# Optimization experiments

Measured on AMD Instinct MI355X. Metric: run time of the kernel, lower is better.

Reference implementation:

```python
import jax, jax.numpy as jnp
import numpy as np

TAU = 2.0       # spikingjelly LIFNode default
V_TH = 1.0      # v_threshold default
ALPHA = 2.0     # surrogate.ATan default alpha

@jax.custom_vjp
def atan_spike(x):
    # Heaviside forward, ATan surrogate gradient backward
    return (x >= 0.0).astype(x.dtype)

def _atan_fwd(x):
    return atan_spike(x), x

def _atan_bwd(x, g):
    return (g * (ALPHA / 2.0) / (1.0 + (jnp.pi / 2.0 * ALPHA * x) ** 2),)

atan_spike.defvjp(_atan_fwd, _atan_bwd)

def lif_scan(cur):
    # cur: [T, ...]; LIF with decay_input=True, hard reset to v_reset=0
    def step(v, c):
        v = v + (c - v) / TAU          # charge with decayed input
        s = atan_spike(v - V_TH)       # fire
        v = (1.0 - s) * v              # hard reset (v_reset = 0)
        return v, s
    v0 = jnp.zeros(cur.shape[1:], cur.dtype)
    _, spikes = jax.lax.scan(step, v0, cur)
    return spikes

def setup_inputs() -> dict:
    key = jax.random.key(0)
    k1, k2 = jax.random.split(key, 2)
    T, B, D = 2048, 32, 512
    x = jax.random.normal(k1, (T, B, D), dtype=jnp.float32)
    W = jax.random.normal(k2, (D, D), dtype=jnp.float32) / np.sqrt(D).astype(np.float32)
    b = jnp.zeros((D,), dtype=jnp.float32)
    return {"x": x, "W": W, "b": b}

def reference(x, W, b):
    # x: [T, B, D]
    xs = jnp.stack([x, jnp.flip(x, axis=0)], axis=2)          # [T, B, 2, D]
    cur = jnp.einsum('tbkd,ed->tbke', xs, W) + b              # Linear (y = x W^T + b)
    s = lif_scan(cur)                                          # [T, B, 2, D] spikes
    return s[:, :, 0, :] + jnp.flip(s[:, :, 1, :], axis=0)    # [T, B, D]
```

## Files before the change

### kernel.cpp

```cpp
#include <hip/hip_runtime.h>
#include <cstddef>
#include <cstdint>

#define T_LEN 2048
#define B_SZ  32
#define D_SZ  512
#define BD    (B_SZ * D_SZ)

#define BM  128
#define BN  128
#define LDP 20

__global__ __launch_bounds__(256) void gemm8x8_kernel(
    const float* __restrict__ A,
    const float* __restrict__ W,
    const float* __restrict__ bias,
    float* __restrict__ Y)
{
#pragma clang fp contract(off)
  __shared__ float As[BM][LDP];
  __shared__ float Bs[BN][LDP];

  const int tid = threadIdx.x;
  const int tx  = tid & 15;
  const int ty  = tid >> 4;
  const int m0  = blockIdx.x * BM;
  const int n0  = blockIdx.y * BN;

  const int sr = tid >> 2;
  const int sq = (tid & 3) << 2;

  const float* Ap0 = A + (size_t)(m0 + sr)      * D_SZ + sq;
  const float* Ap1 = A + (size_t)(m0 + 64 + sr) * D_SZ + sq;
  const float* Wp0 = W + (size_t)(n0 + sr)      * D_SZ + sq;
  const float* Wp1 = W + (size_t)(n0 + 64 + sr) * D_SZ + sq;

  float acc[8][8];
#pragma unroll
  for (int i = 0; i < 8; ++i)
#pragma unroll
    for (int j = 0; j < 8; ++j) acc[i][j] = 0.0f;

  float4 pa0 = *(const float4*)(Ap0);
  float4 pa1 = *(const float4*)(Ap1);
  float4 pb0 = *(const float4*)(Wp0);
  float4 pb1 = *(const float4*)(Wp1);

#pragma unroll 1
  for (int k0 = 0; k0 < D_SZ; k0 += 16) {
    __syncthreads();
    *(float4*)&As[sr][sq]      = pa0;
    *(float4*)&As[64 + sr][sq] = pa1;
    *(float4*)&Bs[sr][sq]      = pb0;
    *(float4*)&Bs[64 + sr][sq] = pb1;
    __syncthreads();

    if (k0 + 16 < D_SZ) {
      pa0 = *(const float4*)(Ap0 + k0 + 16);
      pa1 = *(const float4*)(Ap1 + k0 + 16);
      pb0 = *(const float4*)(Wp0 + k0 + 16);
      pb1 = *(const float4*)(Wp1 + k0 + 16);
    }

#pragma unroll
    for (int kq = 0; kq < 4; ++kq) {
      float4 b[8];
#pragma unroll
      for (int j = 0; j < 8; ++j)
        b[j] = *(const float4*)&Bs[tx + 16 * j][kq << 2];
#pragma unroll
      for (int i = 0; i < 8; ++i) {
        const float4 a = *(const float4*)&As[ty + 16 * i][kq << 2];
#pragma unroll
        for (int j = 0; j < 8; ++j) {
          acc[i][j] = fmaf(a.x, b[j].x, acc[i][j]);
          acc[i][j] = fmaf(a.y, b[j].y, acc[i][j]);
          acc[i][j] = fmaf(a.z, b[j].z, acc[i][j]);
          acc[i][j] = fmaf(a.w, b[j].w, acc[i][j]);
        }
      }
    }
  }

#pragma unroll
  for (int i = 0; i < 8; ++i) {
    const int m = m0 + ty + 16 * i;
#pragma unroll
    for (int j = 0; j < 8; ++j) {
      const int n = n0 + tx + 16 * j;
      Y[(size_t)m * D_SZ + n] = acc[i][j] + bias[n];
    }
  }
}

__global__ __launch_bounds__(64) void scan_dirs_kernel(
    const float* __restrict__ Y,
    uint32_t* __restrict__ bits_f,
    uint32_t* __restrict__ bits_b)
{
#pragma clang fp contract(off)
  const int blk = blockIdx.x;
  const bool fwd = blk < 256;
  const int idx = ((fwd ? blk : blk - 256) << 6) + threadIdx.x;
  float v = 0.0f;

  if (fwd) {
#pragma unroll 1
    for (int g = 0; g < 64; ++g) {
      float c[32];
#pragma unroll
      for (int j = 0; j < 32; ++j)
        c[j] = Y[(size_t)(g * 32 + j) * BD + idx];
      uint32_t w = 0;
#pragma unroll
      for (int j = 0; j < 32; ++j) {
        v = v + (c[j] - v) * 0.5f;
        const bool s = (v - 1.0f) >= 0.0f;
        w |= (uint32_t)s << j;
        v = s ? 0.0f : v;
      }
      bits_f[g * BD + idx] = w;
    }
  } else {
#pragma unroll 1
    for (int g = 63; g >= 0; --g) {
      float c[32];
#pragma unroll
      for (int j = 0; j < 32; ++j)
        c[j] = Y[(size_t)(g * 32 + j) * BD + idx];
      uint32_t w = 0;
#pragma unroll
      for (int j = 31; j >= 0; --j) {
        v = v + (c[j] - v) * 0.5f;
        const bool s = (v - 1.0f) >= 0.0f;
        w |= (uint32_t)s << j;
        v = s ? 0.0f : v;
      }
      bits_b[g * BD + idx] = w;
    }
  }
}

__global__ __launch_bounds__(256) void combine_kernel(
    const uint32_t* __restrict__ bf,
    const uint32_t* __restrict__ bb,
    float* __restrict__ out)
{
  const int gid = blockIdx.x * 256 + threadIdx.x;
  const int f0  = gid << 2;
  const int t   = f0 / BD;
  const int i0  = f0 & (BD - 1);
  const int g   = t >> 5;
  const int bit = t & 31;
  const uint4 wf = *(const uint4*)(bf + g * BD + i0);
  const uint4 wb = *(const uint4*)(bb + g * BD + i0);
  float4 r;
  r.x = (float)(((wf.x >> bit) & 1u) + ((wb.x >> bit) & 1u));
  r.y = (float)(((wf.y >> bit) & 1u) + ((wb.y >> bit) & 1u));
  r.z = (float)(((wf.z >> bit) & 1u) + ((wb.z >> bit) & 1u));
  r.w = (float)(((wf.w >> bit) & 1u) + ((wb.w >> bit) & 1u));
  *(float4*)(out + (size_t)f0) = r;
}

__global__ __launch_bounds__(64) void lif_fwd_kernel(
    const float* __restrict__ Y, float* __restrict__ out,
    int tlen, float* __restrict__ vstate, int carry)
{
#pragma clang fp contract(off)
  const int idx = blockIdx.x * 64 + threadIdx.x;
  float v = carry ? vstate[idx] : 0.0f;
#pragma unroll 16
  for (int t = 0; t < tlen; ++t) {
    const float c = Y[(size_t)t * BD + idx];
    v = v + (c - v) * 0.5f;
    const bool s = (v - 1.0f) >= 0.0f;
    out[(size_t)t * BD + idx] = s ? 1.0f : 0.0f;
    v = s ? 0.0f : v;
  }
  vstate[idx] = v;
}

__global__ __launch_bounds__(64) void lif_bwd_kernel(
    const float* __restrict__ Y, float* __restrict__ out,
    int tlen, float* __restrict__ vstate, int carry)
{
#pragma clang fp contract(off)
  const int idx = blockIdx.x * 64 + threadIdx.x;
  float v = carry ? vstate[idx] : 0.0f;
#pragma unroll 16
  for (int tt = 0; tt < tlen; ++tt) {
    const size_t t = (size_t)(tlen - 1 - tt);
    const float c = Y[t * BD + idx];
    v = v + (c - v) * 0.5f;
    const bool s = (v - 1.0f) >= 0.0f;
    out[t * BD + idx] += s ? 1.0f : 0.0f;
    v = s ? 0.0f : v;
  }
  vstate[idx] = v;
}

extern "C" void kernel_launch(void* const* d_in, const int* in_sizes, int n_in,
                              void* d_out, int out_size, void* d_ws, size_t ws_size,
                              hipStream_t stream)
{
  const float* x = (const float*)d_in[0];
  const float* W = (const float*)d_in[1];
  const float* b = (const float*)d_in[2];
  float* out = (float*)d_out;

  const size_t full_bytes = (size_t)T_LEN * BD * sizeof(float);
  const size_t bit_bytes  = (size_t)(T_LEN / 32) * BD * sizeof(uint32_t);
  const size_t vbytes     = (size_t)BD * sizeof(float);

  if (ws_size >= full_bytes + 2 * bit_bytes) {
    float*    Y  = (float*)d_ws;
    uint32_t* bf = (uint32_t*)((char*)d_ws + full_bytes);
    uint32_t* bb = (uint32_t*)((char*)d_ws + full_bytes + bit_bytes);
    dim3 grid(T_LEN * B_SZ / BM, D_SZ / BN);
    gemm8x8_kernel<<<grid, 256, 0, stream>>>(x, W, b, Y);
    scan_dirs_kernel<<<512, 64, 0, stream>>>(Y, bf, bb);
    combine_kernel<<<(T_LEN * BD / 4) / 256, 256, 0, stream>>>(bf, bb, out);
  } else if (ws_size >= full_bytes + vbytes) {
    float* Y      = (float*)d_ws;
    float* vstate = (float*)((char*)d_ws + full_bytes);
    dim3 grid(T_LEN * B_SZ / BM, D_SZ / BN);
    gemm8x8_kernel<<<grid, 256, 0, stream>>>(x, W, b, Y);
    lif_fwd_kernel<<<BD / 64, 64, 0, stream>>>(Y, out, T_LEN, vstate, 0);
    lif_bwd_kernel<<<BD / 64, 64, 0, stream>>>(Y, out, T_LEN, vstate, 0);
  } else {
    const size_t avail = ws_size > vbytes ? ws_size - vbytes : 0;
    int Tc = T_LEN;
    while (Tc > 4 && (size_t)Tc * BD * sizeof(float) > avail) Tc >>= 1;
    float* Y      = (float*)d_ws;
    float* vstate = (float*)((char*)d_ws + (size_t)Tc * BD * sizeof(float));

    int first = 1;
    for (int t0 = 0; t0 < T_LEN; t0 += Tc) {
      dim3 grid(Tc * B_SZ / BM, D_SZ / BN);
      gemm8x8_kernel<<<grid, 256, 0, stream>>>(x + (size_t)t0 * BD, W, b, Y);
      lif_fwd_kernel<<<BD / 64, 64, 0, stream>>>(Y, out + (size_t)t0 * BD, Tc,
                                                 vstate, first ? 0 : 1);
      first = 0;
    }
    first = 1;
    for (int t0 = T_LEN - Tc; t0 >= 0; t0 -= Tc) {
      dim3 grid(Tc * B_SZ / BM, D_SZ / BN);
      gemm8x8_kernel<<<grid, 256, 0, stream>>>(x + (size_t)t0 * BD, W, b, Y);
      lif_bwd_kernel<<<BD / 64, 64, 0, stream>>>(Y, out + (size_t)t0 * BD, Tc,
                                                 vstate, first ? 0 : 1);
      first = 0;
    }
  }
}
```

Before: 707.3 us.

## Chunk LIF scan over time with warmup, fuse combine, double-buffer GEMM

The bidirectional LIF scan is split into 16 time chunks of 128 steps. Each chunk rebuilds its starting membrane state by running a 128-step warmup from zero over the neighbouring chunk, relying on the 0.5 decay to wash out the unknown initial state. Spikes are written straight to the output, so the separate bit-combine kernel and the bit buffers go away. This raises scan parallelism well above the previous 512 blocks of 64 threads, at the cost of reading Y redundantly during warmup and a small risk of threshold differences. The GEMM now double-buffers LDS, loads A directly into LDS with global_load_lds, and remaps block indices across the XCDs.

```diff
diff --git a/kernel.cpp b/kernel.cpp
--- a/kernel.cpp
+++ b/kernel.cpp
@@ -7,9 +7,12 @@
 #define D_SZ  512
 #define BD    (B_SZ * D_SZ)
 
-#define BM  128
-#define BN  128
-#define LDP 20
+#define BM   128
+#define BN   128
+#define LDPB 20
+
+typedef const __attribute__((address_space(1))) uint32_t* gas1_t;
+typedef __attribute__((address_space(3))) uint32_t* las3_t;
 
 __global__ __launch_bounds__(256) void gemm8x8_kernel(
     const float* __restrict__ A,
@@ -18,68 +21,90 @@
     float* __restrict__ Y)
 {
 #pragma clang fp contract(off)
-  __shared__ float As[BM][LDP];
-  __shared__ float Bs[BN][LDP];
+  __shared__ float As[2][BM * 16];
+  __shared__ float Bs[2][BN][LDPB];
 
   const int tid = threadIdx.x;
   const int tx  = tid & 15;
   const int ty  = tid >> 4;
-  const int m0  = blockIdx.x * BM;
-  const int n0  = blockIdx.y * BN;
+
+  const int nwg  = (int)(gridDim.x * gridDim.y);
+  const int orig = (int)(blockIdx.y * gridDim.x + blockIdx.x);
+  const int q    = nwg >> 3, r = nwg & 7;
+  const int xcd  = orig & 7, loc = orig >> 3;
+  const int tix  = (xcd < r ? xcd * (q + 1) : r * (q + 1) + (xcd - r) * q) + loc;
+  const int m0   = (tix >> 2) * BM;
+  const int n0   = (tix & 3) * BN;
 
   const int sr = tid >> 2;
   const int sq = (tid & 3) << 2;
-
-  const float* Ap0 = A + (size_t)(m0 + sr)      * D_SZ + sq;
-  const float* Ap1 = A + (size_t)(m0 + 64 + sr) * D_SZ + sq;
   const float* Wp0 = W + (size_t)(n0 + sr)      * D_SZ + sq;
   const float* Wp1 = W + (size_t)(n0 + 64 + sr) * D_SZ + sq;
 
+  const int lane = tid & 63;
+  const int wid  = tid >> 6;
+  const int rloc = lane >> 2;
+  const int q4   = (lane & 3) << 2;
+  const int sA0  = 2 * wid, sA1 = 2 * wid + 1;
+  const int oS0  = sA0 * 256, oS1 = sA1 * 256;
+  const float* gA0 = A + (size_t)(m0 + sA0 * 16 + rloc) * D_SZ + q4;
+  const float* gA1 = A + (size_t)(m0 + sA1 * 16 + rloc) * D_SZ + q4;
+
   float acc[8][8];
 #pragma unroll
   for (int i = 0; i < 8; ++i)
 #pragma unroll
     for (int j = 0; j < 8; ++j) acc[i][j] = 0.0f;
 
-  float4 pa0 = *(const float4*)(Ap0);
-  float4 pa1 = *(const float4*)(Ap1);
+  __builtin_amdgcn_global_load_lds((gas1_t)(const void*)gA0,
+                                   (las3_t)(void*)(&As[0][oS0]), 16, 0, 0);
+  __builtin_amdgcn_global_load_lds((gas1_t)(const void*)gA1,
+                                   (las3_t)(void*)(&As[0][oS1]), 16, 0, 0);
   float4 pb0 = *(const float4*)(Wp0);
   float4 pb1 = *(const float4*)(Wp1);
+  *(float4*)&Bs[0][sr][sq]      = pb0;
+  *(float4*)&Bs[0][64 + sr][sq] = pb1;
+  pb0 = *(const float4*)(Wp0 + 16);
+  pb1 = *(const float4*)(Wp1 + 16);
+  __syncthreads();
 
 #pragma unroll 1
-  for (int k0 = 0; k0 < D_SZ; k0 += 16) {
+  for (int kc = 0; kc < 32; ++kc) {
+    const int cur = kc & 1;
+    const int nxt = cur ^ 1;
+    if (kc + 1 < 32) {
+      const int koff = (kc + 1) * 16;
+      __builtin_amdgcn_global_load_lds((gas1_t)(const void*)(gA0 + koff),
+                                       (las3_t)(void*)(&As[nxt][oS0]), 16, 0, 0);
+      __builtin_amdgcn_global_load_lds((gas1_t)(const void*)(gA1 + koff),
+                                       (las3_t)(void*)(&As[nxt][oS1]), 16, 0, 0);
+      *(float4*)&Bs[nxt][sr][sq]      = pb0;
+      *(float4*)&Bs[nxt][64 + sr][sq] = pb1;
+      if (kc + 2 < 32) {
+        pb0 = *(const float4*)(Wp0 + (kc + 2) * 16);
+        pb1 = *(const float4*)(Wp1 + (kc + 2) * 16);
+      }
+    }
+    const float* as = &As[cur][0];
+#pragma unroll
+    for (int kq = 0; kq < 4; ++kq) {
+      float4 bfr[8];
+#pragma unroll
+      for (int j = 0; j < 8; ++j)
+        bfr[j] = *(const float4*)&Bs[cur][tx + 16 * j][kq << 2];
+#pragma unroll
+      for (int i = 0; i < 8; ++i) {
+        const float4 a = *(const float4*)&as[(ty + 16 * i) * 16 + (kq << 2)];
+#pragma unroll
+        for (int j = 0; j < 8; ++j) {
+          acc[i][j] = fmaf(a.x, bfr[j].x, acc[i][j]);
+          acc[i][j] = fmaf(a.y, bfr[j].y, acc[i][j]);
+          acc[i][j] = fmaf(a.z, bfr[j].z, acc[i][j]);
+          acc[i][j] = fmaf(a.w, bfr[j].w, acc[i][j]);
+        }
+      }
+    }
     __syncthreads();
-    *(float4*)&As[sr][sq]      = pa0;
-    *(float4*)&As[64 + sr][sq] = pa1;
-    *(float4*)&Bs[sr][sq]      = pb0;
-    *(float4*)&Bs[64 + sr][sq] = pb1;
-    __syncthreads();
-
-    if (k0 + 16 < D_SZ) {
-      pa0 = *(const float4*)(Ap0 + k0 + 16);
-      pa1 = *(const float4*)(Ap1 + k0 + 16);
-      pb0 = *(const float4*)(Wp0 + k0 + 16);
-      pb1 = *(const float4*)(Wp1 + k0 + 16);
-    }
-
-#pragma unroll
-    for (int kq = 0; kq < 4; ++kq) {
-      float4 b[8];
-#pragma unroll
-      for (int j = 0; j < 8; ++j)
-        b[j] = *(const float4*)&Bs[tx + 16 * j][kq << 2];
-#pragma unroll
-      for (int i = 0; i < 8; ++i) {
-        const float4 a = *(const float4*)&As[ty + 16 * i][kq << 2];
-#pragma unroll
-        for (int j = 0; j < 8; ++j) {
-          acc[i][j] = fmaf(a.x, b[j].x, acc[i][j]);
-          acc[i][j] = fmaf(a.y, b[j].y, acc[i][j]);
-          acc[i][j] = fmaf(a.z, b[j].z, acc[i][j]);
-          acc[i][j] = fmaf(a.w, b[j].w, acc[i][j]);
-        }
-      }
-    }
   }
 
 #pragma unroll
@@ -93,73 +118,92 @@
   }
 }
 
-__global__ __launch_bounds__(64) void scan_dirs_kernel(
+#define CHK  16
+#define CLEN 128
+
+__global__ __launch_bounds__(64) void scan_chunk_kernel(
     const float* __restrict__ Y,
-    uint32_t* __restrict__ bits_f,
-    uint32_t* __restrict__ bits_b)
-{
-#pragma clang fp contract(off)
-  const int blk = blockIdx.x;
-  const bool fwd = blk < 256;
-  const int idx = ((fwd ? blk : blk - 256) << 6) + threadIdx.x;
-  float v = 0.0f;
-
-  if (fwd) {
+    float* __restrict__ out)
+{
+#pragma clang fp contract(off)
+  const int idx = blockIdx.x * 64 + threadIdx.x;
+  const int c   = blockIdx.y;
+  const int t0  = c * CLEN;
+  float creg[32];
+  uint32_t sf0, sf1, sf2, sf3, sb0, sb1, sb2, sb3;
+  float v;
+
+#define LOAD32(TB)                                                            \
+  _Pragma("unroll")                                                           \
+  for (int j = 0; j < 32; ++j) creg[j] = Y[(size_t)((TB) + j) * BD + idx];
+
+  v = 0.0f;
+  if (c > 0) {
 #pragma unroll 1
-    for (int g = 0; g < 64; ++g) {
-      float c[32];
-#pragma unroll
-      for (int j = 0; j < 32; ++j)
-        c[j] = Y[(size_t)(g * 32 + j) * BD + idx];
-      uint32_t w = 0;
+    for (int g = 0; g < 4; ++g) {
+      LOAD32(t0 - 128 + g * 32)
 #pragma unroll
       for (int j = 0; j < 32; ++j) {
-        v = v + (c[j] - v) * 0.5f;
+        v = v + (creg[j] - v) * 0.5f;
         const bool s = (v - 1.0f) >= 0.0f;
-        w |= (uint32_t)s << j;
         v = s ? 0.0f : v;
       }
-      bits_f[g * BD + idx] = w;
-    }
-  } else {
+    }
+  }
+#define FGRP(SF, G)                                                           \
+  {                                                                           \
+    LOAD32(t0 + (G) * 32)                                                     \
+    uint32_t w = 0;                                                           \
+    _Pragma("unroll")                                                         \
+    for (int j = 0; j < 32; ++j) {                                            \
+      v = v + (creg[j] - v) * 0.5f;                                           \
+      const bool s = (v - 1.0f) >= 0.0f;                                      \
+      w |= (uint32_t)s << j;                                                  \
+      v = s ? 0.0f : v;                                                       \
+    }                                                                         \
+    SF = w;                                                                   \
+  }
+  FGRP(sf0, 0) FGRP(sf1, 1) FGRP(sf2, 2) FGRP(sf3, 3)
+
+  v = 0.0f;
+  if (c < CHK - 1) {
 #pragma unroll 1
-    for (int g = 63; g >= 0; --g) {
-      float c[32];
-#pragma unroll
-      for (int j = 0; j < 32; ++j)
-        c[j] = Y[(size_t)(g * 32 + j) * BD + idx];
-      uint32_t w = 0;
+    for (int g = 3; g >= 0; --g) {
+      LOAD32(t0 + 128 + g * 32)
 #pragma unroll
       for (int j = 31; j >= 0; --j) {
-        v = v + (c[j] - v) * 0.5f;
+        v = v + (creg[j] - v) * 0.5f;
         const bool s = (v - 1.0f) >= 0.0f;
-        w |= (uint32_t)s << j;
         v = s ? 0.0f : v;
       }
-      bits_b[g * BD + idx] = w;
-    }
-  }
-}
-
-__global__ __launch_bounds__(256) void combine_kernel(
-    const uint32_t* __restrict__ bf,
-    const uint32_t* __restrict__ bb,
-    float* __restrict__ out)
-{
-  const int gid = blockIdx.x * 256 + threadIdx.x;
-  const int f0  = gid << 2;
-  const int t   = f0 / BD;
-  const int i0  = f0 & (BD - 1);
-  const int g   = t >> 5;
-  const int bit = t & 31;
-  const uint4 wf = *(const uint4*)(bf + g * BD + i0);
-  const uint4 wb = *(const uint4*)(bb + g * BD + i0);
-  float4 r;
-  r.x = (float)(((wf.x >> bit) & 1u) + ((wb.x >> bit) & 1u));
-  r.y = (float)(((wf.y >> bit) & 1u) + ((wb.y >> bit) & 1u));
-  r.z = (float)(((wf.z >> bit) & 1u) + ((wb.z >> bit) & 1u));
-  r.w = (float)(((wf.w >> bit) & 1u) + ((wb.w >> bit) & 1u));
-  *(float4*)(out + (size_t)f0) = r;
+    }
+  }
+#define BGRP(SB, G)                                                           \
+  {                                                                           \
+    LOAD32(t0 + (G) * 32)                                                     \
+    uint32_t w = 0;                                                           \
+    _Pragma("unroll")                                                         \
+    for (int j = 31; j >= 0; --j) {                                           \
+      v = v + (creg[j] - v) * 0.5f;                                           \
+      const bool s = (v - 1.0f) >= 0.0f;                                      \
+      w |= (uint32_t)s << j;                                                  \
+      v = s ? 0.0f : v;                                                       \
+    }                                                                         \
+    SB = w;                                                                   \
+  }
+  BGRP(sb3, 3) BGRP(sb2, 2) BGRP(sb1, 1) BGRP(sb0, 0)
+
+#define WGRP(SF, SB, G)                                                       \
+  _Pragma("unroll")                                                           \
+  for (int j = 0; j < 32; ++j)                                                \
+    out[(size_t)(t0 + (G) * 32 + j) * BD + idx] =                             \
+        (float)(((SF >> j) & 1u) + ((SB >> j) & 1u));
+  WGRP(sf0, sb0, 0) WGRP(sf1, sb1, 1) WGRP(sf2, sb2, 2) WGRP(sf3, sb3, 3)
+
+#undef LOAD32
+#undef FGRP
+#undef BGRP
+#undef WGRP
 }
 
 __global__ __launch_bounds__(64) void lif_fwd_kernel(
@@ -209,24 +253,13 @@
   float* out = (float*)d_out;
 
   const size_t full_bytes = (size_t)T_LEN * BD * sizeof(float);
-  const size_t bit_bytes  = (size_t)(T_LEN / 32) * BD * sizeof(uint32_t);
   const size_t vbytes     = (size_t)BD * sizeof(float);
 
-  if (ws_size >= full_bytes + 2 * bit_bytes) {
-    float*    Y  = (float*)d_ws;
-    uint32_t* bf = (uint32_t*)((char*)d_ws + full_bytes);
-    uint32_t* bb = (uint32_t*)((char*)d_ws + full_bytes + bit_bytes);
+  if (ws_size >= full_bytes) {
+    float* Y = (float*)d_ws;
     dim3 grid(T_LEN * B_SZ / BM, D_SZ / BN);
     gemm8x8_kernel<<<grid, 256, 0, stream>>>(x, W, b, Y);
-    scan_dirs_kernel<<<512, 64, 0, stream>>>(Y, bf, bb);
-    combine_kernel<<<(T_LEN * BD / 4) / 256, 256, 0, stream>>>(bf, bb, out);
-  } else if (ws_size >= full_bytes + vbytes) {
-    float* Y      = (float*)d_ws;
-    float* vstate = (float*)((char*)d_ws + full_bytes);
-    dim3 grid(T_LEN * B_SZ / BM, D_SZ / BN);
-    gemm8x8_kernel<<<grid, 256, 0, stream>>>(x, W, b, Y);
-    lif_fwd_kernel<<<BD / 64, 64, 0, stream>>>(Y, out, T_LEN, vstate, 0);
-    lif_bwd_kernel<<<BD / 64, 64, 0, stream>>>(Y, out, T_LEN, vstate, 0);
+    scan_chunk_kernel<<<dim3(BD / 64, CHK), 64, 0, stream>>>(Y, out);
   } else {
     const size_t avail = ws_size > vbytes ? ws_size - vbytes : 0;
     int Tc = T_LEN;
```

New measurement: 713.4 us. No clear change (+0.9%).
